# Performance work log

Measured on AMD Instinct MI355X. Metric: run time of the kernel, lower is better.

The kernel has to match this reference:

```python
import jax, jax.numpy as jnp
import numpy as np

G = 8          # deformable groups
K = 9          # 3x3 kernel points
MAXR = 10.0    # max_residue_magnitude


def conv2d(x, w, b):
    # x: [B,Cin,H,W], w: [Cout,Cin,3,3], SAME padding, stride 1
    y = jax.lax.conv_general_dilated(x, w, (1, 1), ((1, 1), (1, 1)),
                                     dimension_numbers=('NCHW', 'OIHW', 'NCHW'))
    return y + b[None, :, None, None]


def lrelu(x):
    return jnp.where(x >= 0, x, 0.1 * x)


def offset_branch(x, ws, bs):
    for w, b in zip(ws[:-1], bs[:-1]):
        x = lrelu(conv2d(x, w, b))
    return conv2d(x, ws[-1], bs[-1])


def mdcn(x, offset, mask, w, b):
    # Modulated deformable conv, 3x3, stride 1, pad 1, dilation 1, groups=1.
    # offset: [B, G*K*2, H, W] ordered (g, k, (y,x)); mask: [B, G*K, H, W]
    B, C, H, W = x.shape
    Cg = C // G
    off = offset.reshape(B, G, K, 2, H, W)
    m = mask.reshape(B, G, K, H, W)
    ky = (jnp.arange(K) // 3 - 1).astype(x.dtype)   # kernel dy, pad=1
    kx = (jnp.arange(K) % 3 - 1).astype(x.dtype)    # kernel dx
    hy = jnp.arange(H, dtype=x.dtype)
    wx = jnp.arange(W, dtype=x.dtype)
    py = hy[None, None, None, :, None] + ky[None, None, :, None, None] + off[:, :, :, 0]  # [B,G,K,H,W]
    px = wx[None, None, None, None, :] + kx[None, None, :, None, None] + off[:, :, :, 1]
    y0f = jnp.floor(py); x0f = jnp.floor(px)
    ly = py - y0f; lx = px - x0f
    y0 = y0f.astype(jnp.int32); x0 = x0f.astype(jnp.int32)
    xf = x.reshape(B, G, Cg, H * W)

    def gather(yi, xi):
        valid = ((yi >= 0) & (yi < H) & (xi >= 0) & (xi < W)).astype(x.dtype)
        yc = jnp.clip(yi, 0, H - 1)
        xc = jnp.clip(xi, 0, W - 1)
        idx = (yc * W + xc).reshape(B, G, 1, K * H * W)
        v = jnp.take_along_axis(xf, idx, axis=3).reshape(B, G, Cg, K, H, W)
        return v * valid.reshape(B, G, 1, K, H, W)

    ly_ = ly[:, :, None]; lx_ = lx[:, :, None]  # [B,G,1,K,H,W]
    samp = (gather(y0, x0) * (1 - ly_) * (1 - lx_)
            + gather(y0, x0 + 1) * (1 - ly_) * lx_
            + gather(y0 + 1, x0) * ly_ * (1 - lx_)
            + gather(y0 + 1, x0 + 1) * ly_ * lx_)
    samp = samp * m[:, :, None]                 # modulation
    wr = w.reshape(w.shape[0], G, Cg, K)        # [Cout,G,Cg,K]
    return jnp.einsum('ogck,bgckhw->bohw', wr, samp) + b[None, :, None, None]


def setup_inputs():
    key = jax.random.key(0)
    ks = jax.random.split(key, 40)
    B, C, H, W = 1, 64, 256, 256
    s = 0.05
    inp = {
        'feat_prev': jax.random.normal(ks[0], (B, C, H, W), jnp.float32),
        'feat_next': jax.random.normal(ks[1], (B, C, H, W), jnp.float32),
        'extra_feat_prev': jax.random.normal(ks[2], (B, 2 * C, H, W), jnp.float32),
        'extra_feat_next': jax.random.normal(ks[3], (B, 2 * C, H, W), jnp.float32),
        'flow_prev': jax.random.normal(ks[4], (B, 2, H, W), jnp.float32),
        'flow_next': jax.random.normal(ks[5], (B, 2, H, W), jnp.float32),
    }
    shapes = [(C, 2 * C, 3, 3), (C, C, 3, 3), (C, C, 3, 3), (27 * G, C, 3, 3)]
    i = 6
    for pre in ('off1', 'off2'):
        for j, sh in enumerate(shapes):
            inp[f'{pre}_w{j}'] = jax.random.normal(ks[i], sh, jnp.float32) * s; i += 1
            inp[f'{pre}_b{j}'] = jax.random.normal(ks[i], (sh[0],), jnp.float32) * s; i += 1
    inp['dcn1_w'] = jax.random.normal(ks[i], (C, C, 3, 3), jnp.float32) * s; i += 1
    inp['dcn1_b'] = jax.random.normal(ks[i], (C,), jnp.float32) * s; i += 1
    inp['dcn2_w'] = jax.random.normal(ks[i], (C, C, 3, 3), jnp.float32) * s; i += 1
    inp['dcn2_b'] = jax.random.normal(ks[i], (C,), jnp.float32) * s; i += 1
    inp['fus_w'] = jax.random.normal(ks[i], (C, 2 * C, 3, 3), jnp.float32) * s; i += 1
    inp['fus_b'] = jax.random.normal(ks[i], (C,), jnp.float32) * s
    return inp


def reference(feat_prev, feat_next, extra_feat_prev, extra_feat_next, flow_prev, flow_next,
              off1_w0, off1_b0, off1_w1, off1_b1, off1_w2, off1_b2, off1_w3, off1_b3,
              off2_w0, off2_b0, off2_w1, off2_b1, off2_w2, off2_b2, off2_w3, off2_b3,
              dcn1_w, dcn1_b, dcn2_w, dcn2_b, fus_w, fus_b):
    def branch(feat, extra, flow, ws, bs, dw, db):
        out = offset_branch(extra, ws, bs)
        o1, o2, msk = jnp.split(out, 3, axis=1)
        off = MAXR * jnp.tanh(jnp.concatenate([o1, o2], axis=1))
        off = off + jnp.tile(flow[:, ::-1], (1, off.shape[1] // 2, 1, 1))  # flip(1).repeat
        msk = jax.nn.sigmoid(msk)
        return mdcn(feat, off, msk, dw, db)

    fp = branch(feat_prev, extra_feat_prev, flow_prev,
                [off1_w0, off1_w1, off1_w2, off1_w3], [off1_b0, off1_b1, off1_b2, off1_b3],
                dcn1_w, dcn1_b)
    fn = branch(feat_next, extra_feat_next, flow_next,
                [off2_w0, off2_w1, off2_w2, off2_w3], [off2_b0, off2_b1, off2_b2, off2_b3],
                dcn2_w, dcn2_b)
    return conv2d(jnp.concatenate([fp, fn], axis=1), fus_w, fus_b)
```

## Files before the change

### kernel.cpp

```cpp
#include <hip/hip_runtime.h>
#include <cstddef>
#include <cstdint>

constexpr int IMG = 256;
constexpr int NPIX = 65536;
constexpr int PW = 258;
constexpr size_t PREC = (size_t)PW * PW;

typedef _Float16 h8 __attribute__((ext_vector_type(8)));
typedef float f32x4 __attribute__((ext_vector_type(4)));

template<int CIN>
__device__ __forceinline__ void zero_pad_rec(int i, _Float16* buf)
{
  constexpr int Q = CIN / 8;
  if (i >= 1028 * Q) return;
  int pr = i / Q, qi = i - pr * Q;
  int rec;
  if (pr < 258) rec = pr;
  else if (pr < 516) rec = 257 * 258 + (pr - 258);
  else { int j = pr - 516; rec = (1 + (j >> 1)) * 258 + ((j & 1) ? 257 : 0); }
  *reinterpret_cast<uint4*>(&buf[(size_t)rec * CIN + qi * 8]) = uint4{0, 0, 0, 0};
}

template<int CIN>
__global__ __launch_bounds__(256) void zeropad_k(_Float16* __restrict__ buf)
{
  zero_pad_rec<CIN>(blockIdx.x * 256 + threadIdx.x, buf);
}

template<int CIN>
__global__ __launch_bounds__(256) void prep_hwc_k(
    const float* __restrict__ in, _Float16* __restrict__ out)
{
  int b = blockIdx.x;
  if (b >= 256) { zero_pad_rec<CIN>((b - 256) * 256 + threadIdx.x, out); return; }
  int pix = b * 256 + threadIdx.x;
  int py = pix >> 8, px = pix & 255;
  size_t rec = ((size_t)(py + 1) * PW + px + 1) * CIN;
#pragma unroll
  for (int c0 = 0; c0 < CIN; c0 += 8) {
    _Float16 t[8];
#pragma unroll
    for (int j = 0; j < 8; ++j)
      t[j] = (_Float16)in[(size_t)(c0 + j) * NPIX + pix];
    *reinterpret_cast<uint4*>(&out[rec + c0]) = *reinterpret_cast<uint4*>(t);
  }
}

__device__ __forceinline__ void wfrag(
    const float* __restrict__ w, int cin_tot, int cin_off, int KC, int NBF,
    int nvalid, int idx, _Float16* __restrict__ oHi, _Float16* __restrict__ oLo)
{
  int l = idx & 63;
  int r = idx >> 6;
  int fg = r % NBF; r /= NBF;
  int c = r % KC;
  int t = r / KC;
  int n = fg * 16 + (l & 15);
  int cinb = c * 32 + (l >> 4) * 8;
  _Float16 vh[8], vl[8];
#pragma unroll
  for (int j = 0; j < 8; ++j) {
    float x = 0.f;
    if (n < nvalid) x = w[((size_t)n * cin_tot + cin_off + cinb + j) * 9 + t];
    vh[j] = (_Float16)x;
    vl[j] = (_Float16)(x - (float)vh[j]);
  }
  *reinterpret_cast<uint4*>(oHi + (size_t)idx * 8) = *reinterpret_cast<uint4*>(vh);
  if (oLo)
    *reinterpret_cast<uint4*>(oLo + (size_t)idx * 8) = *reinterpret_cast<uint4*>(vl);
}

__global__ __launch_bounds__(256) void wprep_all_k(
    const float* __restrict__ w0, const float* __restrict__ w1,
    const float* __restrict__ w2, const float* __restrict__ w3,
    const float* __restrict__ wf, int wf_cin_off, const float* __restrict__ dw,
    _Float16* b0h, _Float16* b0l, _Float16* b1h, _Float16* b1l,
    _Float16* b2h, _Float16* b2l, _Float16* b3h, _Float16* b3l,
    _Float16* bfh, _Float16* __restrict__ wB)
{
  int idx = blockIdx.x * 256 + threadIdx.x;
  if (idx < 9216)       wfrag(w0, 128, 0, 4, 4, 64, idx, b0h, b0l);
  else if (idx < 13824) wfrag(w1, 64, 0, 2, 4, 64, idx - 9216, b1h, b1l);
  else if (idx < 18432) wfrag(w2, 64, 0, 2, 4, 64, idx - 13824, b2h, b2l);
  else if (idx < 36864) wfrag(w3, 64, 0, 2, 16, 216, idx - 18432, b3h, b3l);
  else if (idx < 41472) wfrag(wf, 128, wf_cin_off, 2, 4, 64, idx - 36864, bfh, nullptr);
  else if (idx < 46080) {
    int i = idx - 41472;
    int l = i & 63;
    int r = i >> 6;
    int f = r & 3;
    int p = r >> 2;
    int t = p * 4 + (l >> 4);
    int g = (t * 57) >> 9;
    int k = t - 9 * g;
    int n = f * 16 + (l & 15);
    _Float16 v[8];
#pragma unroll
    for (int j = 0; j < 8; ++j)
      v[j] = (_Float16)dw[(size_t)n * 576 + g * 72 + j * 9 + k];
    *reinterpret_cast<uint4*>(wB + (size_t)i * 8) = *reinterpret_cast<uint4*>(v);
  }
}

template<int CIN, int EPI, bool DBL, typename OT>
__global__ __launch_bounds__(128) void conv_mfma_k(
    const _Float16* __restrict__ act, const _Float16* __restrict__ wHi,
    const _Float16* __restrict__ wLo, const float* __restrict__ bias,
    OT* __restrict__ out, int ncout, int NBF)
{
  constexpr int Q = CIN / 8;
  constexpr int KC = CIN / 32;
  constexpr int NT = DBL ? 2 : 1;
  constexpr int NREC = 198;
  __shared__ __align__(16) _Float16 sA[NREC * CIN];

  const int tid = threadIdx.x;
  const int lane = tid & 63;
  const int wv = tid >> 6;
  const int b = blockIdx.x;
  const int inner = b >> 3;
  const int y = (b & 7) * 32 + (inner & 31);
  const int x0 = (inner >> 5) << 6;
  const int n0 = blockIdx.y << 6;

  for (int i = tid; i < NREC * Q; i += 128) {
    int rec = i / Q, q = i - rec * Q;
    int seg = rec / 66, xr = rec - seg * 66;
    size_t g = ((size_t)(y + seg) * PW + x0 + xr) * CIN + q * 8;
    int slot = (q + rec) & (Q - 1);
    *reinterpret_cast<uint4*>(&sA[rec * CIN + slot * 8]) =
        *reinterpret_cast<const uint4*>(&act[g]);
  }

  const int fgb = (n0 >> 4) + wv * 2;
  auto bload = [&](int t, int c, int nf, const _Float16* src) {
    return *reinterpret_cast<const h8*>(
        &src[((((size_t)t * KC + c) * NBF + fgb + nf) * 64 + lane) * 8]);
  };
  h8 Bn[KC][2][NT];
#pragma unroll
  for (int c = 0; c < KC; ++c)
#pragma unroll
    for (int nf = 0; nf < 2; ++nf) {
      Bn[c][nf][0] = bload(0, c, nf, wHi);
      if (DBL) Bn[c][nf][1] = bload(0, c, nf, wLo);
    }

  f32x4 acc[4][2];
#pragma unroll
  for (int a = 0; a < 4; ++a)
#pragma unroll
    for (int n = 0; n < 2; ++n) acc[a][n] = f32x4{0.f, 0.f, 0.f, 0.f};
  __syncthreads();

  const int m = lane & 15, kq = lane >> 4;
#pragma unroll 1
  for (int t = 0; t < 9; ++t) {
    h8 Bc[KC][2][NT];
#pragma unroll
    for (int c = 0; c < KC; ++c)
#pragma unroll
      for (int nf = 0; nf < 2; ++nf) {
        Bc[c][nf][0] = Bn[c][nf][0];
        if (DBL) Bc[c][nf][1] = Bn[c][nf][1];
      }
    if (t < 8) {
#pragma unroll
      for (int c = 0; c < KC; ++c)
#pragma unroll
        for (int nf = 0; nf < 2; ++nf) {
          Bn[c][nf][0] = bload(t + 1, c, nf, wHi);
          if (DBL) Bn[c][nf][1] = bload(t + 1, c, nf, wLo);
        }
    }
    const int lrb = (t / 3) * 66 + (t % 3) + m;
#pragma unroll
    for (int c = 0; c < KC; ++c) {
      const int q = c * 4 + kq;
#pragma unroll
      for (int mf = 0; mf < 4; ++mf) {
        int lr = lrb + mf * 16;
        int slot = (q + lr) & (Q - 1);
        h8 ah = *reinterpret_cast<const h8*>(&sA[lr * CIN + slot * 8]);
#pragma unroll
        for (int nf = 0; nf < 2; ++nf) {
          acc[mf][nf] = __builtin_amdgcn_mfma_f32_16x16x32_f16(
              ah, Bc[c][nf][0], acc[mf][nf], 0, 0, 0);
          if (DBL)
            acc[mf][nf] = __builtin_amdgcn_mfma_f32_16x16x32_f16(
                ah, Bc[c][nf][1], acc[mf][nf], 0, 0, 0);
        }
      }
    }
  }

  if (EPI == 0) {
#pragma unroll
    for (int nf = 0; nf < 2; ++nf) {
      const int ch = wv * 32 + nf * 16 + m;
      const float bv = bias[ch];
#pragma unroll
      for (int mf = 0; mf < 4; ++mf)
#pragma unroll
        for (int r = 0; r < 4; ++r) {
          int p = mf * 16 + kq * 4 + r;
          float v = acc[mf][nf][r] + bv;
          v = (v >= 0.f) ? v : 0.1f * v;
          reinterpret_cast<_Float16*>(out)[((size_t)(y + 1) * PW + x0 + p + 1) * 64 + ch] =
              (_Float16)v;
        }
    }
  } else {
    __syncthreads();
    float* sF = reinterpret_cast<float*>(sA);
#pragma unroll
    for (int mf = 0; mf < 4; ++mf)
#pragma unroll
      for (int nf = 0; nf < 2; ++nf) {
        int ml = mf * 16 + kq * 4;
        int nl = wv * 32 + nf * 16 + m;
        f32x4 v = acc[mf][nf];
        if (EPI == 1) {
          float bv = (n0 + nl < ncout) ? bias[n0 + nl] : 0.f;
          v[0] += bv; v[1] += bv; v[2] += bv; v[3] += bv;
        }
        *reinterpret_cast<f32x4*>(&sF[nl * 68 + ml]) = v;
      }
    __syncthreads();
    for (int i = tid; i < 1024; i += 128) {
      int row = i >> 4, cx = (i & 15) * 4;
      int gc = n0 + row;
      if (gc < ncout) {
        f32x4 v = *reinterpret_cast<f32x4*>(&sF[row * 68 + cx]);
        size_t ob = (size_t)gc * NPIX + (size_t)y * IMG + x0 + cx;
        if (EPI == 2) {
          float* op = reinterpret_cast<float*>(out) + ob;
          op[0] += v[0]; op[1] += v[1]; op[2] += v[2]; op[3] += v[3];
        } else if (sizeof(OT) == 2) {
          _Float16 t4[4] = {(_Float16)v[0], (_Float16)v[1],
                            (_Float16)v[2], (_Float16)v[3]};
          *reinterpret_cast<uint2*>(reinterpret_cast<_Float16*>(out) + ob) =
              *reinterpret_cast<uint2*>(t4);
        } else {
          *reinterpret_cast<f32x4*>(reinterpret_cast<float*>(out) + ob) = v;
        }
      }
    }
  }
}

__global__ __launch_bounds__(256) void featg_k(
    const float* __restrict__ in, _Float16* __restrict__ out)
{
  int pix = blockIdx.x * 256 + threadIdx.x;
#pragma unroll
  for (int g = 0; g < 8; ++g) {
    _Float16 t[8];
#pragma unroll
    for (int c = 0; c < 8; ++c)
      t[c] = (_Float16)in[(size_t)(g * 8 + c) * NPIX + pix];
    *reinterpret_cast<uint4*>(&out[((size_t)g * NPIX + pix) * 8]) =
        *reinterpret_cast<uint4*>(t);
  }
}

__global__ __launch_bounds__(256, 4) void mdcn_mfma_k(
    const _Float16* __restrict__ featG, const _Float16* __restrict__ o216,
    const float* __restrict__ flow, const _Float16* __restrict__ wB,
    const float* __restrict__ bias, _Float16* __restrict__ actF)
{
  const int tid = threadIdx.x;
  const int lane = tid & 63;
  const int wv = tid >> 6;
  const int b = blockIdx.x;
  const int inner = b >> 3;
  const int row = (b & 7) * 32 + (inner & 31);
  const int xseg = inner >> 5;
  const int m = lane & 15;
  const int tq = lane >> 4;
  const int xw = xseg * 64 + wv * 16;
  const int x = xw + m;
  const int pix = row * 256 + x;

  const float fy = flow[NPIX + pix];
  const float fx = flow[pix];

  f32x4 acc[4];
#pragma unroll
  for (int f = 0; f < 4; ++f) acc[f] = f32x4{0.f, 0.f, 0.f, 0.f};

  auto rawload = [&](int p, float& a0, float& a1, float& a2) {
    int t = p * 4 + tq;
    int g = (t * 57) >> 9;
    int k = t - 9 * g;
    a0 = (float)o216[(size_t)(g * 18 + 2 * k) * NPIX + pix];
    a1 = (float)o216[(size_t)(g * 18 + 2 * k + 1) * NPIX + pix];
    a2 = (float)o216[(size_t)(144 + g * 9 + k) * NPIX + pix];
  };

  float c0, c1, c2;
  rawload(0, c0, c1, c2);

#pragma unroll 1
  for (int p = 0; p < 18; ++p) {
    float n0 = 0.f, n1 = 0.f, n2 = 0.f;
    if (p < 17) rawload(p + 1, n0, n1, n2);

    const int t = p * 4 + tq;
    const int g = (t * 57) >> 9;
    const int k = t - 9 * g;
    const float mm = 1.f / (1.f + __expf(-c2));
    const float pyf = (float)row + (float)(k / 3 - 1) + 10.f * tanhf(c0) + fy;
    const float pxf = (float)x + (float)(k % 3 - 1) + 10.f * tanhf(c1) + fx;
    const float y0f = floorf(pyf), x0f = floorf(pxf);
    const float ly = pyf - y0f, lx = pxf - x0f;
    const int y0 = (int)y0f, x0i = (int)x0f;
    const int y1 = y0 + 1, x1 = x0i + 1;
    const bool vy0 = (unsigned)y0 < (unsigned)IMG, vy1 = (unsigned)y1 < (unsigned)IMG;
    const bool vx0 = (unsigned)x0i < (unsigned)IMG, vx1 = (unsigned)x1 < (unsigned)IMG;
    const int y0c = min(max(y0, 0), IMG - 1), y1c = min(max(y1, 0), IMG - 1);
    const int x0c = min(max(x0i, 0), IMG - 1), x1c = min(max(x1, 0), IMG - 1);
    const float w00 = (vy0 && vx0) ? (1.f - ly) * (1.f - lx) * mm : 0.f;
    const float w01 = (vy0 && vx1) ? (1.f - ly) * lx * mm : 0.f;
    const float w10 = (vy1 && vx0) ? ly * (1.f - lx) * mm : 0.f;
    const float w11 = (vy1 && vx1) ? ly * lx * mm : 0.f;

    const _Float16* fg = featG + ((size_t)g << 19);
    h8 ga = *reinterpret_cast<const h8*>(fg + (size_t)(y0c * IMG + x0c) * 8);
    h8 gb = *reinterpret_cast<const h8*>(fg + (size_t)(y0c * IMG + x1c) * 8);
    h8 gc = *reinterpret_cast<const h8*>(fg + (size_t)(y1c * IMG + x0c) * 8);
    h8 gd = *reinterpret_cast<const h8*>(fg + (size_t)(y1c * IMG + x1c) * 8);

    h8 af;
#pragma unroll
    for (int j = 0; j < 8; ++j)
      af[j] = (_Float16)(w00 * (float)ga[j] + w01 * (float)gb[j] +
                         w10 * (float)gc[j] + w11 * (float)gd[j]);

    const _Float16* wp = wB + ((size_t)p * 256 + lane) * 8;
#pragma unroll
    for (int f = 0; f < 4; ++f) {
      h8 bf = *reinterpret_cast<const h8*>(wp + (size_t)f * 512);
      acc[f] = __builtin_amdgcn_mfma_f32_16x16x32_f16(af, bf, acc[f], 0, 0, 0);
    }
    c0 = n0; c1 = n1; c2 = n2;
  }

  const size_t rb = ((size_t)(row + 1) * PW + xw + 1) * 64;
#pragma unroll
  for (int f = 0; f < 4; ++f) {
    const int ch = f * 16 + m;
    const float bv = bias[ch];
#pragma unroll
    for (int r = 0; r < 4; ++r)
      actF[rb + (size_t)(tq * 4 + r) * 64 + ch] = (_Float16)(acc[f][r] + bv);
  }
}

extern "C" void kernel_launch(void* const* d_in, const int* in_sizes, int n_in,
                              void* d_out, int out_size, void* d_ws, size_t ws_size,
                              hipStream_t stream)
{
  const float* feat[2]  = {(const float*)d_in[0], (const float*)d_in[1]};
  const float* extra[2] = {(const float*)d_in[2], (const float*)d_in[3]};
  const float* flow[2]  = {(const float*)d_in[4], (const float*)d_in[5]};
  const float* ow[2][4];
  const float* ob[2][4];
  for (int br = 0; br < 2; ++br)
    for (int j = 0; j < 4; ++j) {
      ow[br][j] = (const float*)d_in[6 + br * 8 + j * 2];
      ob[br][j] = (const float*)d_in[6 + br * 8 + j * 2 + 1];
    }
  const float* dcnw[2] = {(const float*)d_in[22], (const float*)d_in[24]};
  const float* dcnb[2] = {(const float*)d_in[23], (const float*)d_in[25]};
  const float* fusw = (const float*)d_in[26];
  const float* fusb = (const float*)d_in[27];

  char* wsb = (char*)d_ws;
  size_t off = 0;
  auto alloc = [&](size_t bytes) {
    void* p = wsb + off;
    off += (bytes + 255) & ~(size_t)255;
    return p;
  };
  _Float16* actI = (_Float16*)alloc(PREC * 128 * 2);
  _Float16* actA = (_Float16*)alloc(PREC * 64 * 2);
  _Float16* actB = (_Float16*)alloc(PREC * 64 * 2);
  _Float16* actF = (_Float16*)alloc(PREC * 64 * 2);
  _Float16* o216 = (_Float16*)alloc((size_t)216 * NPIX * 2);
  _Float16* featG = (_Float16*)alloc((size_t)8 * NPIX * 8 * 2);
  _Float16* wB = (_Float16*)alloc(36864 * 2);
  _Float16* wb0h = (_Float16*)alloc(147456); _Float16* wb0l = (_Float16*)alloc(147456);
  _Float16* wb1h = (_Float16*)alloc(73728);  _Float16* wb1l = (_Float16*)alloc(73728);
  _Float16* wb2h = (_Float16*)alloc(73728);  _Float16* wb2l = (_Float16*)alloc(73728);
  _Float16* wb3h = (_Float16*)alloc(294912); _Float16* wb3l = (_Float16*)alloc(294912);
  _Float16* wbFh = (_Float16*)alloc(73728);
  float* outp = (float*)d_out;

  dim3 blk256(256), blk128(128);
  zeropad_k<64><<<dim3(33), blk256, 0, stream>>>(actA);
  zeropad_k<64><<<dim3(33), blk256, 0, stream>>>(actB);
  zeropad_k<64><<<dim3(33), blk256, 0, stream>>>(actF);

  for (int br = 0; br < 2; ++br) {
    prep_hwc_k<128><<<dim3(321), blk256, 0, stream>>>(extra[br], actI);
    wprep_all_k<<<dim3(180), blk256, 0, stream>>>(
        ow[br][0], ow[br][1], ow[br][2], ow[br][3], fusw, br * 64, dcnw[br],
        wb0h, wb0l, wb1h, wb1l, wb2h, wb2l, wb3h, wb3l, wbFh, wB);

    conv_mfma_k<128, 0, true, _Float16><<<dim3(1024, 1), blk128, 0, stream>>>(
        actI, wb0h, wb0l, ob[br][0], actA, 64, 4);
    conv_mfma_k<64, 0, true, _Float16><<<dim3(1024, 1), blk128, 0, stream>>>(
        actA, wb1h, wb1l, ob[br][1], actB, 64, 4);
    conv_mfma_k<64, 0, true, _Float16><<<dim3(1024, 1), blk128, 0, stream>>>(
        actB, wb2h, wb2l, ob[br][2], actA, 64, 4);
    conv_mfma_k<64, 1, true, _Float16><<<dim3(1024, 4), blk128, 0, stream>>>(
        actA, wb3h, wb3l, ob[br][3], o216, 216, 16);

    featg_k<<<dim3(256), blk256, 0, stream>>>(feat[br], featG);
    mdcn_mfma_k<<<dim3(1024), blk256, 0, stream>>>(
        featG, o216, flow[br], wB, dcnb[br], actF);

    if (br == 0)
      conv_mfma_k<64, 1, false, float><<<dim3(1024, 1), blk128, 0, stream>>>(
          actF, wbFh, nullptr, fusb, outp, 64, 4);
    else
      conv_mfma_k<64, 2, false, float><<<dim3(1024, 1), blk128, 0, stream>>>(
          actF, wbFh, nullptr, nullptr, outp, 64, 4);
  }
}
```

Baseline: 558.7 us.

## Software-pipeline deformable gathers one step ahead and use fast tanh/sigmoid math

The deformable-conv kernel now computes sampling coordinates and issues the four bilinear feature gathers for step p+1 while the MFMAs of step p run, with raw offset loads prefetched two steps ahead. Gather latency was previously exposed each iteration. It also replaces tanhf and the sigmoid division with exp and rcp intrinsics, and does the bilinear blend in fp16 with fp16 weights. The cost is higher register pressure from double-buffered gather vectors and reduced precision in the interpolation.

New measurement: 540.8 us. 3.2% less time.

```diff
diff --git a/kernel.cpp b/kernel.cpp
--- a/kernel.cpp
+++ b/kernel.cpp
@@ -286,6 +286,7 @@
 
   const float fy = flow[NPIX + pix];
   const float fx = flow[pix];
+  const float rowf = (float)row, xf = (float)x;
 
   f32x4 acc[4];
 #pragma unroll
@@ -300,20 +301,21 @@
     a2 = (float)o216[(size_t)(144 + g * 9 + k) * NPIX + pix];
   };
 
-  float c0, c1, c2;
-  rawload(0, c0, c1, c2);
-
-#pragma unroll 1
-  for (int p = 0; p < 18; ++p) {
-    float n0 = 0.f, n1 = 0.f, n2 = 0.f;
-    if (p < 17) rawload(p + 1, n0, n1, n2);
-
+  auto setup = [&](int p, float s0, float s1, float s2,
+                   _Float16& h00, _Float16& h01, _Float16& h10, _Float16& h11,
+                   h8& A, h8& B, h8& C, h8& D) {
     const int t = p * 4 + tq;
     const int g = (t * 57) >> 9;
     const int k = t - 9 * g;
-    const float mm = 1.f / (1.f + __expf(-c2));
-    const float pyf = (float)row + (float)(k / 3 - 1) + 10.f * tanhf(c0) + fy;
-    const float pxf = (float)x + (float)(k % 3 - 1) + 10.f * tanhf(c1) + fx;
+    const int kd = (k * 11) >> 5;
+    const int km = k - 3 * kd;
+    const float mm = __builtin_amdgcn_rcpf(1.f + __expf(-s2));
+    const float e0 = __expf(2.f * s0);
+    const float e1 = __expf(2.f * s1);
+    const float th0 = 1.f - 2.f * __builtin_amdgcn_rcpf(e0 + 1.f);
+    const float th1 = 1.f - 2.f * __builtin_amdgcn_rcpf(e1 + 1.f);
+    const float pyf = rowf + (float)(kd - 1) + 10.f * th0 + fy;
+    const float pxf = xf + (float)(km - 1) + 10.f * th1 + fx;
     const float y0f = floorf(pyf), x0f = floorf(pxf);
     const float ly = pyf - y0f, lx = pxf - x0f;
     const int y0 = (int)y0f, x0i = (int)x0f;
@@ -322,30 +324,52 @@
     const bool vx0 = (unsigned)x0i < (unsigned)IMG, vx1 = (unsigned)x1 < (unsigned)IMG;
     const int y0c = min(max(y0, 0), IMG - 1), y1c = min(max(y1, 0), IMG - 1);
     const int x0c = min(max(x0i, 0), IMG - 1), x1c = min(max(x1, 0), IMG - 1);
-    const float w00 = (vy0 && vx0) ? (1.f - ly) * (1.f - lx) * mm : 0.f;
-    const float w01 = (vy0 && vx1) ? (1.f - ly) * lx * mm : 0.f;
-    const float w10 = (vy1 && vx0) ? ly * (1.f - lx) * mm : 0.f;
-    const float w11 = (vy1 && vx1) ? ly * lx * mm : 0.f;
-
+    const float oy = 1.f - ly, ox = 1.f - lx;
+    const float py0 = oy * mm, py1 = ly * mm;
+    const float w00 = (vy0 && vx0) ? py0 * ox : 0.f;
+    const float w01 = (vy0 && vx1) ? py0 * lx : 0.f;
+    const float w10 = (vy1 && vx0) ? py1 * ox : 0.f;
+    const float w11 = (vy1 && vx1) ? py1 * lx : 0.f;
+    h00 = (_Float16)w00; h01 = (_Float16)w01;
+    h10 = (_Float16)w10; h11 = (_Float16)w11;
     const _Float16* fg = featG + ((size_t)g << 19);
-    h8 ga = *reinterpret_cast<const h8*>(fg + (size_t)(y0c * IMG + x0c) * 8);
-    h8 gb = *reinterpret_cast<const h8*>(fg + (size_t)(y0c * IMG + x1c) * 8);
-    h8 gc = *reinterpret_cast<const h8*>(fg + (size_t)(y1c * IMG + x0c) * 8);
-    h8 gd = *reinterpret_cast<const h8*>(fg + (size_t)(y1c * IMG + x1c) * 8);
+    A = *reinterpret_cast<const h8*>(fg + (size_t)(y0c * IMG + x0c) * 8);
+    B = *reinterpret_cast<const h8*>(fg + (size_t)(y0c * IMG + x1c) * 8);
+    C = *reinterpret_cast<const h8*>(fg + (size_t)(y1c * IMG + x0c) * 8);
+    D = *reinterpret_cast<const h8*>(fg + (size_t)(y1c * IMG + x1c) * 8);
+  };
+
+  float r0, r1, r2, s0, s1, s2;
+  _Float16 h00, h01, h10, h11, v00, v01, v10, v11;
+  h8 ga, gb, gc, gd, na, nb, nc, nd;
+
+  rawload(0, s0, s1, s2);
+  setup(0, s0, s1, s2, h00, h01, h10, h11, ga, gb, gc, gd);
+  rawload(1, r0, r1, r2);
+
+#pragma unroll 1
+  for (int p = 0; p < 18; ++p) {
+    if (p < 17) setup(p + 1, r0, r1, r2, v00, v01, v10, v11, na, nb, nc, nd);
+    if (p < 16) rawload(p + 2, r0, r1, r2);
+
+    const _Float16* wp = wB + ((size_t)p * 256 + lane) * 8;
+    h8 bf0 = *reinterpret_cast<const h8*>(wp);
+    h8 bf1 = *reinterpret_cast<const h8*>(wp + 512);
+    h8 bf2 = *reinterpret_cast<const h8*>(wp + 1024);
+    h8 bf3 = *reinterpret_cast<const h8*>(wp + 1536);
 
     h8 af;
 #pragma unroll
     for (int j = 0; j < 8; ++j)
-      af[j] = (_Float16)(w00 * (float)ga[j] + w01 * (float)gb[j] +
-                         w10 * (float)gc[j] + w11 * (float)gd[j]);
-
-    const _Float16* wp = wB + ((size_t)p * 256 + lane) * 8;
-#pragma unroll
-    for (int f = 0; f < 4; ++f) {
-      h8 bf = *reinterpret_cast<const h8*>(wp + (size_t)f * 512);
-      acc[f] = __builtin_amdgcn_mfma_f32_16x16x32_f16(af, bf, acc[f], 0, 0, 0);
-    }
-    c0 = n0; c1 = n1; c2 = n2;
+      af[j] = (_Float16)(ga[j] * h00 + gb[j] * h01 + gc[j] * h10 + gd[j] * h11);
+
+    acc[0] = __builtin_amdgcn_mfma_f32_16x16x32_f16(af, bf0, acc[0], 0, 0, 0);
+    acc[1] = __builtin_amdgcn_mfma_f32_16x16x32_f16(af, bf1, acc[1], 0, 0, 0);
+    acc[2] = __builtin_amdgcn_mfma_f32_16x16x32_f16(af, bf2, acc[2], 0, 0, 0);
+    acc[3] = __builtin_amdgcn_mfma_f32_16x16x32_f16(af, bf3, acc[3], 0, 0, 0);
+
+    ga = na; gb = nb; gc = nc; gd = nd;
+    h00 = v00; h01 = v01; h10 = v10; h11 = v11;
   }
 
   const size_t rb = ((size_t)(row + 1) * PW + xw + 1) * 64;
```
